# Performance work log

Hardware: AMD Instinct MI355X
Metric: run time of the kernel (lower is better)

Reference implementation:

```python
import jax, jax.numpy as jnp
import numpy as np

EMBED_DIM = 1024
NUM_HEADS = 16
HEAD_DIM = EMBED_DIM // NUM_HEADS
CACHE_LEN = 16384


def setup_inputs() -> dict:
    key = jax.random.key(0)
    ks = jax.random.split(key, 10)
    s = 1.0 / np.sqrt(EMBED_DIM)
    return {
        "x": jax.random.normal(ks[0], (EMBED_DIM,), dtype=jnp.float32),
        "vk_cache": jax.random.normal(ks[1], (2, CACHE_LEN, NUM_HEADS, HEAD_DIM), dtype=jnp.float32),
        "Wv": jax.random.normal(ks[2], (EMBED_DIM, EMBED_DIM), dtype=jnp.float32) * s,
        "bv": jnp.zeros((EMBED_DIM,), dtype=jnp.float32),
        "Wq": jax.random.normal(ks[3], (EMBED_DIM, EMBED_DIM), dtype=jnp.float32) * s,
        "bq": jnp.zeros((EMBED_DIM,), dtype=jnp.float32),
        "Wk": jax.random.normal(ks[4], (EMBED_DIM, EMBED_DIM), dtype=jnp.float32) * s,
        "bk": jnp.zeros((EMBED_DIM,), dtype=jnp.float32),
        "Wo": jax.random.normal(ks[5], (EMBED_DIM, EMBED_DIM), dtype=jnp.float32) * s,
        "bo": jnp.zeros((EMBED_DIM,), dtype=jnp.float32),
    }


def reference(x, vk_cache, Wv, bv, Wq, bq, Wk, bk, Wo, bo):
    # Project single token to q/k/v
    v_i = (x @ Wv + bv).reshape(1, NUM_HEADS, HEAD_DIM)
    q_i = (x @ Wq + bq).reshape(NUM_HEADS, HEAD_DIM)
    k_i = (x @ Wk + bk).reshape(1, NUM_HEADS, HEAD_DIM)
    # Shift cache left by one, append new token   -> (CACHE_LEN, H, D)
    v = jnp.concatenate((vk_cache[0, 1:], v_i), axis=0)
    k = jnp.concatenate((vk_cache[1, 1:], k_i), axis=0)
    # Valid positions = any nonzero value entry
    mask = jnp.any(v != 0, axis=(1, 2))  # (CACHE_LEN,)
    # Scaled dot-product attention for the single query
    att = jnp.einsum('hd,khd->hk', q_i, k) / jnp.sqrt(jnp.float32(HEAD_DIM))
    att = jnp.where(mask, att, -jnp.inf)
    att = jax.nn.softmax(att, axis=-1)
    values = jnp.einsum('hk,khd->hd', att, v).reshape(EMBED_DIM)
    out_i = values @ Wo + bo
    return (out_i, jnp.stack([v, k]))
```

## Files before the change

kernel.cpp:

```cpp
#include <hip/hip_runtime.h>
#include <math.h>

#define EMBED 1024
#define NHEAD 16
#define HDIM  64
#define CLEN  16384

#define WS_QKV   0
#define WS_QP    3072
#define WS_PM    199680
#define WS_PL    216064
#define WS_PACC  232448
#define WS_GM    1281024
#define WS_GL    1281536
#define WS_GACC  1282048
#define WS_VALS  1314816
#define WS_OPART 1315840

__global__ __launch_bounds__(256) void qkv_proj(
    const float* __restrict__ x,
    const float* __restrict__ Wq,
    const float* __restrict__ Wk,
    const float* __restrict__ Wv,
    float* __restrict__ ws) {
  int m = blockIdx.x >> 6;
  int c = blockIdx.x & 63;
  const float* W = (m == 0) ? Wq : (m == 1) ? Wk : Wv;
  int j = threadIdx.x << 2;
  int i0 = c * 16;
  float4 acc = make_float4(0.f, 0.f, 0.f, 0.f);
  for (int i = i0; i < i0 + 16; ++i) {
    float xv = x[i];
    float4 w = *(const float4*)(W + (size_t)i * EMBED + j);
    acc.x += xv * w.x; acc.y += xv * w.y;
    acc.z += xv * w.z; acc.w += xv * w.w;
  }
  *(float4*)(ws + WS_QP + (size_t)(m * 64 + c) * EMBED + j) = acc;
}

__global__ __launch_bounds__(256) void qkv_reduce(
    const float* __restrict__ bq, const float* __restrict__ bk,
    const float* __restrict__ bv, float* __restrict__ ws) {
  int m = blockIdx.x >> 2;
  int j = ((blockIdx.x & 3) << 8) + threadIdx.x;
  const float* b = (m == 0) ? bq : (m == 1) ? bk : bv;
  float s = b[j];
  const float* p = ws + WS_QP + (size_t)m * 64 * EMBED + j;
  for (int c = 0; c < 64; ++c) s += p[(size_t)c * EMBED];
  ws[WS_QKV + m * EMBED + j] = s;
}

__global__ __launch_bounds__(256) void shift_attn(
    const float* __restrict__ cache,
    float* __restrict__ out,
    float* __restrict__ ws) {
  __shared__ float sacc[4][EMBED];
  __shared__ float sm[4][NHEAD];
  __shared__ float sl[4][NHEAD];

  const int wv   = threadIdx.x >> 6;
  const int lane = threadIdx.x & 63;
  const int h    = lane >> 2;
  const int e    = h * HDIM + ((lane & 3) << 4);

  float qf[16];
#pragma unroll
  for (int j = 0; j < 16; j += 4) {
    float4 t = *(const float4*)(ws + WS_QKV + e + j);
    qf[j] = t.x; qf[j + 1] = t.y; qf[j + 2] = t.z; qf[j + 3] = t.w;
  }

  float mrun = -INFINITY, lsum = 0.f;
  float acc[16];
#pragma unroll
  for (int j = 0; j < 16; ++j) acc[j] = 0.f;

  const float* vin = cache;
  const float* kin = cache + (size_t)CLEN * EMBED;
  float* vout = out + EMBED;
  float* kout = out + EMBED + (size_t)CLEN * EMBED;
  const int t0 = blockIdx.x * 16 + wv * 4;

  for (int it = 0; it < 4; ++it) {
    int t = t0 + it;
    const float* vsrc = (t < CLEN - 1) ? (vin + (size_t)(t + 1) * EMBED + e)
                                       : (ws + WS_QKV + 2 * EMBED + e);
    const float* ksrc = (t < CLEN - 1) ? (kin + (size_t)(t + 1) * EMBED + e)
                                       : (ws + WS_QKV + EMBED + e);
    float vv[16], kk[16];
#pragma unroll
    for (int j = 0; j < 16; j += 4) {
      float4 tv = *(const float4*)(vsrc + j);
      vv[j] = tv.x; vv[j + 1] = tv.y; vv[j + 2] = tv.z; vv[j + 3] = tv.w;
    }
#pragma unroll
    for (int j = 0; j < 16; j += 4) {
      float4 tk = *(const float4*)(ksrc + j);
      kk[j] = tk.x; kk[j + 1] = tk.y; kk[j + 2] = tk.z; kk[j + 3] = tk.w;
    }
    float* vd = vout + (size_t)t * EMBED + e;
    float* kd = kout + (size_t)t * EMBED + e;
#pragma unroll
    for (int j = 0; j < 16; j += 4)
      *(float4*)(vd + j) = make_float4(vv[j], vv[j + 1], vv[j + 2], vv[j + 3]);
#pragma unroll
    for (int j = 0; j < 16; j += 4)
      *(float4*)(kd + j) = make_float4(kk[j], kk[j + 1], kk[j + 2], kk[j + 3]);

    bool nz = false;
#pragma unroll
    for (int j = 0; j < 16; ++j) nz = nz || (vv[j] != 0.f);
    float dot = 0.f;
#pragma unroll
    for (int j = 0; j < 16; ++j) dot += qf[j] * kk[j];
    dot += __shfl_xor(dot, 1, 64);
    dot += __shfl_xor(dot, 2, 64);

    if (__any((int)nz)) {
      float s  = dot * 0.125f;
      float mn = fmaxf(mrun, s);
      float alpha = __expf(mrun - mn);
      float p     = __expf(s - mn);
      lsum = lsum * alpha + p;
#pragma unroll
      for (int j = 0; j < 16; ++j) acc[j] = acc[j] * alpha + p * vv[j];
      mrun = mn;
    }
  }

  if (wv > 0) {
#pragma unroll
    for (int j = 0; j < 16; j += 4)
      *(float4*)(&sacc[wv][e + j]) =
          make_float4(acc[j], acc[j + 1], acc[j + 2], acc[j + 3]);
    if ((lane & 3) == 0) { sm[wv][h] = mrun; sl[wv][h] = lsum; }
  }
  __syncthreads();
  if (wv == 0) {
    for (int w = 1; w < 4; ++w) {
      float m2 = sm[w][h];
      float M  = fmaxf(mrun, m2);
      float a1 = (mrun == -INFINITY) ? 0.f : __expf(mrun - M);
      float a2 = (m2   == -INFINITY) ? 0.f : __expf(m2 - M);
      lsum = a1 * lsum + a2 * sl[w][h];
#pragma unroll
      for (int j = 0; j < 16; j += 4) {
        float4 av = *(const float4*)(&sacc[w][e + j]);
        acc[j]     = a1 * acc[j]     + a2 * av.x;
        acc[j + 1] = a1 * acc[j + 1] + a2 * av.y;
        acc[j + 2] = a1 * acc[j + 2] + a2 * av.z;
        acc[j + 3] = a1 * acc[j + 3] + a2 * av.w;
      }
      mrun = M;
    }
    if ((lane & 3) == 0) {
      ws[WS_PM + blockIdx.x * NHEAD + h] = mrun;
      ws[WS_PL + blockIdx.x * NHEAD + h] = lsum;
    }
    float* pa = ws + WS_PACC + (size_t)blockIdx.x * EMBED + e;
#pragma unroll
    for (int j = 0; j < 16; j += 4)
      *(float4*)(pa + j) =
          make_float4(acc[j], acc[j + 1], acc[j + 2], acc[j + 3]);
  }
}

__global__ __launch_bounds__(1024) void combine1(float* __restrict__ ws) {
  int g = blockIdx.x, t = threadIdx.x, h = t >> 6;
  int w0 = g * 32;
  float M = -INFINITY;
  for (int w = w0; w < w0 + 32; ++w)
    M = fmaxf(M, ws[WS_PM + w * NHEAD + h]);
  float L = 0.f, a = 0.f;
  for (int w = w0; w < w0 + 32; ++w) {
    float mw = ws[WS_PM + w * NHEAD + h];
    float sc = (mw == -INFINITY) ? 0.f : __expf(mw - M);
    L += sc * ws[WS_PL + w * NHEAD + h];
    a += sc * ws[WS_PACC + (size_t)w * EMBED + t];
  }
  if ((t & 63) == 0) {
    ws[WS_GM + g * NHEAD + h] = M;
    ws[WS_GL + g * NHEAD + h] = L;
  }
  ws[WS_GACC + (size_t)g * EMBED + t] = a;
}

__global__ __launch_bounds__(1024) void combine2(float* __restrict__ ws) {
  int t = threadIdx.x, h = t >> 6;
  float M = -INFINITY;
  for (int g = 0; g < 32; ++g)
    M = fmaxf(M, ws[WS_GM + g * NHEAD + h]);
  float L = 0.f, a = 0.f;
  for (int g = 0; g < 32; ++g) {
    float mg = ws[WS_GM + g * NHEAD + h];
    float sc = (mg == -INFINITY) ? 0.f : __expf(mg - M);
    L += sc * ws[WS_GL + g * NHEAD + h];
    a += sc * ws[WS_GACC + (size_t)g * EMBED + t];
  }
  ws[WS_VALS + t] = a / L;
}

__global__ __launch_bounds__(256) void out_proj(
    const float* __restrict__ ws_in,
    const float* __restrict__ Wo,
    float* __restrict__ ws) {
  int c = blockIdx.x;
  int j = threadIdx.x << 2;
  int i0 = c * 16;
  const float* vals = ws_in + WS_VALS;
  float4 acc = make_float4(0.f, 0.f, 0.f, 0.f);
  for (int i = i0; i < i0 + 16; ++i) {
    float xv = vals[i];
    float4 w = *(const float4*)(Wo + (size_t)i * EMBED + j);
    acc.x += xv * w.x; acc.y += xv * w.y;
    acc.z += xv * w.z; acc.w += xv * w.w;
  }
  *(float4*)(ws + WS_OPART + (size_t)c * EMBED + j) = acc;
}

__global__ __launch_bounds__(1024) void out_reduce(
    const float* __restrict__ ws, const float* __restrict__ bo,
    float* __restrict__ out) {
  int t = threadIdx.x;
  float s = bo[t];
  const float* p = ws + WS_OPART + t;
  for (int c = 0; c < 64; ++c) s += p[(size_t)c * EMBED];
  out[t] = s;
}

extern "C" void kernel_launch(void* const* d_in, const int* in_sizes, int n_in,
                              void* d_out, int out_size, void* d_ws, size_t ws_size,
                              hipStream_t stream) {
  const float* x     = (const float*)d_in[0];
  const float* cache = (const float*)d_in[1];
  const float* Wv    = (const float*)d_in[2];
  const float* bv    = (const float*)d_in[3];
  const float* Wq    = (const float*)d_in[4];
  const float* bq    = (const float*)d_in[5];
  const float* Wk    = (const float*)d_in[6];
  const float* bk    = (const float*)d_in[7];
  const float* Wo    = (const float*)d_in[8];
  const float* bo    = (const float*)d_in[9];
  float* out = (float*)d_out;
  float* ws  = (float*)d_ws;

  qkv_proj  <<<192, 256, 0, stream>>>(x, Wq, Wk, Wv, ws);
  qkv_reduce<<<12, 256, 0, stream>>>(bq, bk, bv, ws);
  shift_attn<<<1024, 256, 0, stream>>>(cache, out, ws);
  combine1  <<<32, 1024, 0, stream>>>(ws);
  combine2  <<<1, 1024, 0, stream>>>(ws);
  out_proj  <<<64, 256, 0, stream>>>(ws, Wo, ws);
  out_reduce<<<1, 1024, 0, stream>>>(ws, bo, out);
}
```

Baseline: 297.6 us.

## Coalesce cache row access across wave and fold final combine into out_proj

The attention kernel now has each lane load four float4 chunks strided by 256 floats, so one wave's loads and stores cover contiguous 1 KB segments instead of each lane reading 64 contiguous bytes. In exchange, each lane tracks four heads with separate running max and sum, and the dot-product reduction uses four shuffle stages over 16 lanes. Separately, the single-block combine2 kernel is removed and its per-head merge is recomputed inside out_proj for the 16 values each block needs, saving one launch at the cost of redundant small reads.

```diff
diff --git a/kernel.cpp b/kernel.cpp
--- a/kernel.cpp
+++ b/kernel.cpp
@@ -14,8 +14,7 @@
 #define WS_GM    1281024
 #define WS_GL    1281536
 #define WS_GACC  1282048
-#define WS_VALS  1314816
-#define WS_OPART 1315840
+#define WS_OPART 1314816
 
 __global__ __launch_bounds__(256) void qkv_proj(
     const float* __restrict__ x,
@@ -54,23 +53,23 @@
     const float* __restrict__ cache,
     float* __restrict__ out,
     float* __restrict__ ws) {
-  __shared__ float sacc[4][EMBED];
+  __shared__ float sacc[3][EMBED];
   __shared__ float sm[4][NHEAD];
   __shared__ float sl[4][NHEAD];
 
   const int wv   = threadIdx.x >> 6;
   const int lane = threadIdx.x & 63;
-  const int h    = lane >> 2;
-  const int e    = h * HDIM + ((lane & 3) << 4);
+  const int grp  = lane >> 4;
 
   float qf[16];
 #pragma unroll
-  for (int j = 0; j < 16; j += 4) {
-    float4 t = *(const float4*)(ws + WS_QKV + e + j);
-    qf[j] = t.x; qf[j + 1] = t.y; qf[j + 2] = t.z; qf[j + 3] = t.w;
-  }
-
-  float mrun = -INFINITY, lsum = 0.f;
+  for (int c = 0; c < 4; ++c) {
+    float4 t = *(const float4*)(ws + WS_QKV + c * 256 + lane * 4);
+    qf[c * 4] = t.x; qf[c * 4 + 1] = t.y; qf[c * 4 + 2] = t.z; qf[c * 4 + 3] = t.w;
+  }
+
+  float m[4] = {-INFINITY, -INFINITY, -INFINITY, -INFINITY};
+  float l[4] = {0.f, 0.f, 0.f, 0.f};
   float acc[16];
 #pragma unroll
   for (int j = 0; j < 16; ++j) acc[j] = 0.f;
@@ -83,85 +82,107 @@
 
   for (int it = 0; it < 4; ++it) {
     int t = t0 + it;
-    const float* vsrc = (t < CLEN - 1) ? (vin + (size_t)(t + 1) * EMBED + e)
-                                       : (ws + WS_QKV + 2 * EMBED + e);
-    const float* ksrc = (t < CLEN - 1) ? (kin + (size_t)(t + 1) * EMBED + e)
-                                       : (ws + WS_QKV + EMBED + e);
+    const float* vsrc = (t < CLEN - 1) ? (vin + (size_t)(t + 1) * EMBED)
+                                       : (ws + WS_QKV + 2 * EMBED);
+    const float* ksrc = (t < CLEN - 1) ? (kin + (size_t)(t + 1) * EMBED)
+                                       : (ws + WS_QKV + EMBED);
     float vv[16], kk[16];
 #pragma unroll
-    for (int j = 0; j < 16; j += 4) {
-      float4 tv = *(const float4*)(vsrc + j);
-      vv[j] = tv.x; vv[j + 1] = tv.y; vv[j + 2] = tv.z; vv[j + 3] = tv.w;
-    }
-#pragma unroll
-    for (int j = 0; j < 16; j += 4) {
-      float4 tk = *(const float4*)(ksrc + j);
-      kk[j] = tk.x; kk[j + 1] = tk.y; kk[j + 2] = tk.z; kk[j + 3] = tk.w;
-    }
-    float* vd = vout + (size_t)t * EMBED + e;
-    float* kd = kout + (size_t)t * EMBED + e;
-#pragma unroll
-    for (int j = 0; j < 16; j += 4)
-      *(float4*)(vd + j) = make_float4(vv[j], vv[j + 1], vv[j + 2], vv[j + 3]);
-#pragma unroll
-    for (int j = 0; j < 16; j += 4)
-      *(float4*)(kd + j) = make_float4(kk[j], kk[j + 1], kk[j + 2], kk[j + 3]);
+    for (int c = 0; c < 4; ++c) {
+      float4 tv = *(const float4*)(vsrc + c * 256 + lane * 4);
+      vv[c * 4] = tv.x; vv[c * 4 + 1] = tv.y; vv[c * 4 + 2] = tv.z; vv[c * 4 + 3] = tv.w;
+    }
+#pragma unroll
+    for (int c = 0; c < 4; ++c) {
+      float4 tk = *(const float4*)(ksrc + c * 256 + lane * 4);
+      kk[c * 4] = tk.x; kk[c * 4 + 1] = tk.y; kk[c * 4 + 2] = tk.z; kk[c * 4 + 3] = tk.w;
+    }
+    float* vd = vout + (size_t)t * EMBED;
+    float* kd = kout + (size_t)t * EMBED;
+#pragma unroll
+    for (int c = 0; c < 4; ++c)
+      *(float4*)(vd + c * 256 + lane * 4) =
+          make_float4(vv[c * 4], vv[c * 4 + 1], vv[c * 4 + 2], vv[c * 4 + 3]);
+#pragma unroll
+    for (int c = 0; c < 4; ++c)
+      *(float4*)(kd + c * 256 + lane * 4) =
+          make_float4(kk[c * 4], kk[c * 4 + 1], kk[c * 4 + 2], kk[c * 4 + 3]);
 
     bool nz = false;
 #pragma unroll
     for (int j = 0; j < 16; ++j) nz = nz || (vv[j] != 0.f);
-    float dot = 0.f;
-#pragma unroll
-    for (int j = 0; j < 16; ++j) dot += qf[j] * kk[j];
-    dot += __shfl_xor(dot, 1, 64);
-    dot += __shfl_xor(dot, 2, 64);
+
+    float d[4];
+#pragma unroll
+    for (int c = 0; c < 4; ++c) {
+      d[c] = qf[c * 4] * kk[c * 4] + qf[c * 4 + 1] * kk[c * 4 + 1] +
+             qf[c * 4 + 2] * kk[c * 4 + 2] + qf[c * 4 + 3] * kk[c * 4 + 3];
+    }
+#pragma unroll
+    for (int msk = 1; msk <= 8; msk <<= 1) {
+#pragma unroll
+      for (int c = 0; c < 4; ++c) d[c] += __shfl_xor(d[c], msk, 64);
+    }
 
     if (__any((int)nz)) {
-      float s  = dot * 0.125f;
-      float mn = fmaxf(mrun, s);
-      float alpha = __expf(mrun - mn);
-      float p     = __expf(s - mn);
-      lsum = lsum * alpha + p;
-#pragma unroll
-      for (int j = 0; j < 16; ++j) acc[j] = acc[j] * alpha + p * vv[j];
-      mrun = mn;
+#pragma unroll
+      for (int c = 0; c < 4; ++c) {
+        float s  = d[c] * 0.125f;
+        float mn = fmaxf(m[c], s);
+        float alpha = __expf(m[c] - mn);
+        float p     = __expf(s - mn);
+        l[c] = l[c] * alpha + p;
+#pragma unroll
+        for (int j = 0; j < 4; ++j)
+          acc[c * 4 + j] = acc[c * 4 + j] * alpha + p * vv[c * 4 + j];
+        m[c] = mn;
+      }
     }
   }
 
   if (wv > 0) {
 #pragma unroll
-    for (int j = 0; j < 16; j += 4)
-      *(float4*)(&sacc[wv][e + j]) =
-          make_float4(acc[j], acc[j + 1], acc[j + 2], acc[j + 3]);
-    if ((lane & 3) == 0) { sm[wv][h] = mrun; sl[wv][h] = lsum; }
+    for (int c = 0; c < 4; ++c)
+      *(float4*)(&sacc[wv - 1][c * 256 + lane * 4]) =
+          make_float4(acc[c * 4], acc[c * 4 + 1], acc[c * 4 + 2], acc[c * 4 + 3]);
+    if ((lane & 15) == 0) {
+#pragma unroll
+      for (int c = 0; c < 4; ++c) {
+        sm[wv][c * 4 + grp] = m[c];
+        sl[wv][c * 4 + grp] = l[c];
+      }
+    }
   }
   __syncthreads();
   if (wv == 0) {
     for (int w = 1; w < 4; ++w) {
-      float m2 = sm[w][h];
-      float M  = fmaxf(mrun, m2);
-      float a1 = (mrun == -INFINITY) ? 0.f : __expf(mrun - M);
-      float a2 = (m2   == -INFINITY) ? 0.f : __expf(m2 - M);
-      lsum = a1 * lsum + a2 * sl[w][h];
-#pragma unroll
-      for (int j = 0; j < 16; j += 4) {
-        float4 av = *(const float4*)(&sacc[w][e + j]);
-        acc[j]     = a1 * acc[j]     + a2 * av.x;
-        acc[j + 1] = a1 * acc[j + 1] + a2 * av.y;
-        acc[j + 2] = a1 * acc[j + 2] + a2 * av.z;
-        acc[j + 3] = a1 * acc[j + 3] + a2 * av.w;
-      }
-      mrun = M;
-    }
-    if ((lane & 3) == 0) {
-      ws[WS_PM + blockIdx.x * NHEAD + h] = mrun;
-      ws[WS_PL + blockIdx.x * NHEAD + h] = lsum;
-    }
-    float* pa = ws + WS_PACC + (size_t)blockIdx.x * EMBED + e;
-#pragma unroll
-    for (int j = 0; j < 16; j += 4)
-      *(float4*)(pa + j) =
-          make_float4(acc[j], acc[j + 1], acc[j + 2], acc[j + 3]);
+#pragma unroll
+      for (int c = 0; c < 4; ++c) {
+        float m2 = sm[w][c * 4 + grp];
+        float M  = fmaxf(m[c], m2);
+        float a1 = (m[c] == -INFINITY) ? 0.f : __expf(m[c] - M);
+        float a2 = (m2   == -INFINITY) ? 0.f : __expf(m2 - M);
+        l[c] = a1 * l[c] + a2 * sl[w][c * 4 + grp];
+        float4 av = *(const float4*)(&sacc[w - 1][c * 256 + lane * 4]);
+        acc[c * 4]     = a1 * acc[c * 4]     + a2 * av.x;
+        acc[c * 4 + 1] = a1 * acc[c * 4 + 1] + a2 * av.y;
+        acc[c * 4 + 2] = a1 * acc[c * 4 + 2] + a2 * av.z;
+        acc[c * 4 + 3] = a1 * acc[c * 4 + 3] + a2 * av.w;
+        m[c] = M;
+      }
+    }
+    if ((lane & 15) == 0) {
+#pragma unroll
+      for (int c = 0; c < 4; ++c) {
+        ws[WS_PM + blockIdx.x * NHEAD + c * 4 + grp] = m[c];
+        ws[WS_PL + blockIdx.x * NHEAD + c * 4 + grp] = l[c];
+      }
+    }
+    float* pa = ws + WS_PACC + (size_t)blockIdx.x * EMBED;
+#pragma unroll
+    for (int c = 0; c < 4; ++c)
+      *(float4*)(pa + c * 256 + lane * 4) =
+          make_float4(acc[c * 4], acc[c * 4 + 1], acc[c * 4 + 2], acc[c * 4 + 3]);
   }
 }
 
@@ -185,33 +206,33 @@
   ws[WS_GACC + (size_t)g * EMBED + t] = a;
 }
 
-__global__ __launch_bounds__(1024) void combine2(float* __restrict__ ws) {
-  int t = threadIdx.x, h = t >> 6;
-  float M = -INFINITY;
-  for (int g = 0; g < 32; ++g)
-    M = fmaxf(M, ws[WS_GM + g * NHEAD + h]);
-  float L = 0.f, a = 0.f;
-  for (int g = 0; g < 32; ++g) {
-    float mg = ws[WS_GM + g * NHEAD + h];
-    float sc = (mg == -INFINITY) ? 0.f : __expf(mg - M);
-    L += sc * ws[WS_GL + g * NHEAD + h];
-    a += sc * ws[WS_GACC + (size_t)g * EMBED + t];
-  }
-  ws[WS_VALS + t] = a / L;
-}
-
 __global__ __launch_bounds__(256) void out_proj(
-    const float* __restrict__ ws_in,
     const float* __restrict__ Wo,
     float* __restrict__ ws) {
+  __shared__ float svals[16];
   int c = blockIdx.x;
+  int i0 = c * 16;
+  int h0 = i0 >> 6;
+  if (threadIdx.x < 16) {
+    int i = i0 + threadIdx.x;
+    float M = -INFINITY;
+    for (int g = 0; g < 32; ++g)
+      M = fmaxf(M, ws[WS_GM + g * NHEAD + h0]);
+    float L = 0.f, a = 0.f;
+    for (int g = 0; g < 32; ++g) {
+      float mg = ws[WS_GM + g * NHEAD + h0];
+      float sc = (mg == -INFINITY) ? 0.f : __expf(mg - M);
+      L += sc * ws[WS_GL + g * NHEAD + h0];
+      a += sc * ws[WS_GACC + (size_t)g * EMBED + i];
+    }
+    svals[threadIdx.x] = a / L;
+  }
+  __syncthreads();
   int j = threadIdx.x << 2;
-  int i0 = c * 16;
-  const float* vals = ws_in + WS_VALS;
   float4 acc = make_float4(0.f, 0.f, 0.f, 0.f);
-  for (int i = i0; i < i0 + 16; ++i) {
-    float xv = vals[i];
-    float4 w = *(const float4*)(Wo + (size_t)i * EMBED + j);
+  for (int i = 0; i < 16; ++i) {
+    float xv = svals[i];
+    float4 w = *(const float4*)(Wo + (size_t)(i0 + i) * EMBED + j);
     acc.x += xv * w.x; acc.y += xv * w.y;
     acc.z += xv * w.z; acc.w += xv * w.w;
   }
@@ -248,7 +269,6 @@
   qkv_reduce<<<12, 256, 0, stream>>>(bq, bk, bv, ws);
   shift_attn<<<1024, 256, 0, stream>>>(cache, out, ws);
   combine1  <<<32, 1024, 0, stream>>>(ws);
-  combine2  <<<1, 1024, 0, stream>>>(ws);
-  out_proj  <<<64, 256, 0, stream>>>(ws, Wo, ws);
+  out_proj  <<<64, 256, 0, stream>>>(Wo, ws);
   out_reduce<<<1, 1024, 0, stream>>>(ws, bo, out);
 }
```

Measured after the change: 291.2 us. -2.1%, faster.
